# Performance work log

Measured on AMD Instinct MI355X. Metric: run time of the kernel, lower is better.

## Reference

```python
import jax, jax.numpy as jnp
import numpy as np

EPS = 1e-5
L0_BETA = 2.0 / 3.0   # unused in deterministic path
L0_GAMMA = -0.1
L0_ZETA = 1.1
NEG_SLOPE = 0.2


def _bn(v, axes, g, b, pshape):
    # batch-norm using batch statistics (training-mode math, biased var like torch)
    mean = jnp.mean(v, axis=axes, keepdims=True)
    var = jnp.var(v, axis=axes, keepdims=True)
    return (v - mean) * jax.lax.rsqrt(var + EPS) * g.reshape(pshape) + b.reshape(pshape)


def setup_inputs() -> dict:
    key = jax.random.key(0)
    ks = jax.random.split(key, 4)
    n, c, t, h, w = 32, 1024, 32, 7, 7
    n_nodes = 128
    return {
        "x": jax.random.normal(ks[0], (n, c, t, h, w), jnp.float32),
        "nodes": jax.random.normal(ks[1], (n_nodes, c), jnp.float32),
        "g1": jnp.ones((c,), jnp.float32), "b1": jnp.zeros((c,), jnp.float32),
        "g2": jnp.ones((c,), jnp.float32), "b2": jnp.zeros((c,), jnp.float32),
        "g3": jnp.ones((n_nodes,), jnp.float32), "b3": jnp.zeros((n_nodes,), jnp.float32),
        "W": jax.random.normal(ks[2], (c, c), jnp.float32) * (1.0 / np.sqrt(c)),
        "bW": jnp.zeros((c,), jnp.float32),
        "loc": jnp.ones((1,), jnp.float32),  # hard-concrete location param (penalty_loc_mean=1)
        "g6": jnp.ones((c,), jnp.float32), "b6": jnp.zeros((c,), jnp.float32),
    }


def reference(x, nodes, g1, b1, g2, b2, g3, b3, W, bW, loc, g6, b6):
    # x: (n,c,t,h,w), nodes: (K,c)
    # bn_1: BatchNorm3d over channel c
    x = _bn(x, (0, 2, 3, 4), g1, b1, (1, -1, 1, 1, 1))
    # bn_2: BatchNorm1d on (K,c) -> per-channel stats across nodes
    nd = _bn(nodes, (0,), g2, b2, (1, -1))
    # linear_1
    nd = nd @ W.T + bW
    # bn_3: pl.BatchNorm(n_nodes, dim=0) -> per-node stats across channels
    nd = _bn(nd, (1,), g3, b3, (-1, 1))
    # tensor_product_1: f (n,h,w,K,t)
    f = jnp.einsum('ncthw,kc->nhwkt', x, nd)
    # L0Norm hard-concrete gate (deterministic/eval path)
    s_bar = jax.nn.sigmoid(loc) * (L0_ZETA - L0_GAMMA) + L0_GAMMA
    gate = jnp.clip(s_bar, 0.0, 1.0)
    alpha = f * gate
    # tensor_product_2: y (n,c,t,h,w)
    y = jnp.einsum('nhwkt,kc->ncthw', alpha, nd)
    # bn_6 + LeakyReLU(0.2)
    y = _bn(y, (0, 2, 3, 4), g6, b6, (1, -1, 1, 1, 1))
    return jnp.where(y >= 0, y, NEG_SLOPE * y)
```

## Files before the change

kernel.cpp:

```cpp
#include <hip/hip_runtime.h>
#include <hip/hip_bf16.h>

#define NB 32
#define CC 1024
#define SS 1568
#define KK 128
#define NCOL 448
#define EPSV 1e-5f
#define XP_P 132
#define NSB3 224

typedef __attribute__((ext_vector_type(8))) short bf16x8;
typedef __attribute__((ext_vector_type(4))) short bf16x4v;
typedef __attribute__((ext_vector_type(4))) float f32x4;

__device__ __forceinline__ unsigned short f2bf(float f) {
  union { float f; unsigned u; } v; v.f = f;
  return (unsigned short)((v.u + 0x7fffu + ((v.u >> 16) & 1u)) >> 16);
}
__device__ __forceinline__ float bf2f(unsigned short h) {
  union { unsigned u; float f; } v; v.u = ((unsigned)h) << 16; return v.f;
}

__global__ __launch_bounds__(256) void xpose_stats(
    const float* __restrict__ x, unsigned short* __restrict__ xT,
    float* __restrict__ p1s, float* __restrict__ p1q) {
  __shared__ float lt[64 * XP_P];
  int sb = blockIdx.x, cc = blockIdx.y, n = blockIdx.z;
  int t = threadIdx.x;
  int s0 = sb * 112, c0 = cc * 64;
  const float* xp = x + ((size_t)n * CC + c0) * SS + s0;
  #pragma unroll
  for (int j = 0; j < 7; j++) {
    int idx = t + 256 * j;
    int r = idx / 28, q = idx % 28;
    float4 v = *(const float4*)(xp + (size_t)r * SS + 4 * q);
    *(float4*)&lt[r * XP_P + 4 * (q ^ (r >> 3))] = v;
  }
  __syncthreads();
  {
    int r = t >> 2, m = t & 3;
    float s = 0.f, sq = 0.f;
    #pragma unroll
    for (int i = 0; i < 7; i++) {
      int b = m * 7 + i;
      float4 v = *(const float4*)&lt[r * XP_P + 4 * (b ^ (r >> 3))];
      s  += v.x + v.y + v.z + v.w;
      sq += v.x * v.x + v.y * v.y + v.z * v.z + v.w * v.w;
    }
    s += __shfl_xor(s, 1); sq += __shfl_xor(sq, 1);
    s += __shfl_xor(s, 2); sq += __shfl_xor(sq, 2);
    if (m == 0) {
      int col = n * 14 + sb;
      p1s[(size_t)(c0 + r) * NCOL + col] = s;
      p1q[(size_t)(c0 + r) * NCOL + col] = sq;
    }
  }
  if (t < 224) {
    int co = t & 7, sl = t >> 3;
    #pragma unroll
    for (int j = 0; j < 4; j++) {
      int sloc = sl + 28 * j;
      int s = s0 + sloc;
      bf16x8 pk;
      #pragma unroll
      for (int i = 0; i < 8; i++) {
        int r = co * 8 + i;
        pk[i] = (short)f2bf(lt[r * XP_P + 4 * ((sloc >> 2) ^ co) + (sloc & 3)]);
      }
      size_t off = (size_t)n * 1605632 +
                   (size_t)((s >> 4) * 32 + (cc * 2 + (co >> 2))) * 512 +
                   (s & 15) * 32 + (co & 3) * 8;
      *(bf16x8*)(xT + off) = pk;
    }
  }
}

__global__ void bn1_fin(const float* __restrict__ p1s, const float* __restrict__ p1q,
                        const float* __restrict__ g1, const float* __restrict__ b1,
                        float* a1, float* c1) {
  __shared__ float red[4][32][2];
  int t = threadIdx.x;
  int cl = t & 31, part = t >> 5, w = t >> 6;
  int c = blockIdx.x * 32 + cl;
  const float4* ps = (const float4*)(p1s + (size_t)c * NCOL + part * 56);
  const float4* pq = (const float4*)(p1q + (size_t)c * NCOL + part * 56);
  float s = 0.f, sq = 0.f;
  #pragma unroll
  for (int i = 0; i < 14; i++) {
    float4 v = ps[i]; s += v.x + v.y + v.z + v.w;
    float4 u = pq[i]; sq += u.x + u.y + u.z + u.w;
  }
  s += __shfl_xor(s, 32); sq += __shfl_xor(sq, 32);
  if ((t & 63) < 32) { red[w][cl][0] = s; red[w][cl][1] = sq; }
  __syncthreads();
  if (t < 32) {
    float st = red[0][t][0] + red[1][t][0] + red[2][t][0] + red[3][t][0];
    float qt = red[0][t][1] + red[1][t][1] + red[2][t][1] + red[3][t][1];
    float inv = 1.f / ((float)NB * SS);
    float m = st * inv, var = qt * inv - m * m;
    float r = rsqrtf(var + EPSV);
    float a = g1[c] * r;
    a1[c] = a; c1[c] = b1[c] - m * a;
  }
}

__global__ void bn2_nh(const float* __restrict__ nodes, const float* __restrict__ g2,
                       const float* __restrict__ b2, unsigned short* __restrict__ nh) {
  __shared__ float sred[4][8][2];
  __shared__ float bc[8][2];
  int t = threadIdx.x;
  int cl = t & 7, kq = t >> 3, w = t >> 6;
  int c = blockIdx.x * 8 + cl;
  float s = 0.f, sq = 0.f;
  #pragma unroll
  for (int i = 0; i < 4; i++) {
    float v = nodes[(size_t)(kq + 32 * i) * CC + c];
    s += v; sq += v * v;
  }
  s += __shfl_xor(s, 8);  sq += __shfl_xor(sq, 8);
  s += __shfl_xor(s, 16); sq += __shfl_xor(sq, 16);
  s += __shfl_xor(s, 32); sq += __shfl_xor(sq, 32);
  if ((t & 63) < 8) { sred[w][cl][0] = s; sred[w][cl][1] = sq; }
  __syncthreads();
  if (t < 8) {
    float st = sred[0][t][0] + sred[1][t][0] + sred[2][t][0] + sred[3][t][0];
    float qt = sred[0][t][1] + sred[1][t][1] + sred[2][t][1] + sred[3][t][1];
    float inv = 1.f / (float)KK;
    float m = st * inv, var = qt * inv - m * m;
    float r = rsqrtf(var + EPSV);
    float a = g2[blockIdx.x * 8 + t] * r;
    bc[t][0] = a; bc[t][1] = b2[blockIdx.x * 8 + t] - m * a;
  }
  __syncthreads();
  float a = bc[cl][0], cc2 = bc[cl][1];
  #pragma unroll
  for (int i = 0; i < 4; i++) {
    int k = kq + 32 * i;
    nh[(size_t)k * CC + c] = f2bf(nodes[(size_t)k * CC + c] * a + cc2);
  }
}

__global__ __launch_bounds__(256) void linear_mfma(
    const unsigned short* __restrict__ nh, const float* __restrict__ Wm,
    const float* __restrict__ bW, float* __restrict__ Lb) {
  int jt = blockIdx.x, mt = blockIdx.y;
  int t = threadIdx.x, w = t >> 6, lane = t & 63, g = lane >> 4, l15 = lane & 15;
  int krow = mt * 64 + w * 16 + l15;
  f32x4 acc[2];
  acc[0] = (f32x4){0.f,0.f,0.f,0.f}; acc[1] = (f32x4){0.f,0.f,0.f,0.f};
  #pragma unroll 4
  for (int c0 = 0; c0 < CC; c0 += 32) {
    bf16x8 af = *(const bf16x8*)(nh + (size_t)krow * CC + c0 + g * 8);
    #pragma unroll
    for (int nf = 0; nf < 2; nf++) {
      const float* wr = Wm + (size_t)(jt * 32 + nf * 16 + l15) * CC + c0 + g * 8;
      float4 v0 = *(const float4*)wr, v1 = *(const float4*)(wr + 4);
      bf16x8 bfr;
      bfr[0] = (short)f2bf(v0.x); bfr[1] = (short)f2bf(v0.y);
      bfr[2] = (short)f2bf(v0.z); bfr[3] = (short)f2bf(v0.w);
      bfr[4] = (short)f2bf(v1.x); bfr[5] = (short)f2bf(v1.y);
      bfr[6] = (short)f2bf(v1.z); bfr[7] = (short)f2bf(v1.w);
      acc[nf] = __builtin_amdgcn_mfma_f32_16x16x32_bf16(af, bfr, acc[nf], 0, 0, 0);
    }
  }
  #pragma unroll
  for (int nf = 0; nf < 2; nf++) {
    int j = jt * 32 + nf * 16 + l15;
    float bwv = bW[j];
    #pragma unroll
    for (int r = 0; r < 4; r++)
      Lb[(size_t)(mt * 64 + w * 16 + g * 4 + r) * CC + j] = acc[nf][r] + bwv;
  }
}

__global__ void bn3_pack(const float* __restrict__ Lb, const float* __restrict__ g3,
                         const float* __restrict__ b3, const float* __restrict__ loc,
                         const float* __restrict__ a1, const float* __restrict__ c1,
                         unsigned short* __restrict__ ndA2, unsigned short* __restrict__ Mt,
                         unsigned short* __restrict__ MtL, float* __restrict__ Cst) {
  __shared__ float red[8];
  int k = blockIdx.x, t = threadIdx.x, w = t >> 6;
  float vv[4];
  float s = 0.f, sq = 0.f;
  for (int i = 0; i < 4; i++) {
    float v = Lb[(size_t)k * CC + t + 256 * i];
    vv[i] = v; s += v; sq += v * v;
  }
  for (int m = 1; m < 64; m <<= 1) { s += __shfl_xor(s, m); sq += __shfl_xor(sq, m); }
  if ((t & 63) == 0) { red[w] = s; red[4 + w] = sq; }
  __syncthreads();
  s  = red[0] + red[1] + red[2] + red[3];
  sq = red[4] + red[5] + red[6] + red[7];
  float inv = 1.f / (float)CC;
  float m3 = s * inv, var = sq * inv - m3 * m3;
  float r = rsqrtf(var + EPSV);
  float a = g3[k] * r, cc3 = b3[k] - m3 * a;
  float lv = loc[0];
  float gate = 1.f / (1.f + __expf(-lv)) * 1.2f - 0.1f;
  gate = fminf(fmaxf(gate, 0.f), 1.f);
  float cs = 0.f;
  for (int i = 0; i < 4; i++) {
    int j = t + 256 * i;
    float nd = vv[i] * a + cc3;
    unsigned short ndb = f2bf(nd * a1[j]);
    unsigned short mtb = f2bf(gate * nd);
    ndA2[(size_t)((k >> 4) * 32 + (j >> 5)) * 512 + (k & 15) * 32 + ((j >> 3) & 3) * 8 + (j & 7)] = ndb;
    Mt[(size_t)((j >> 4) * 4 + (k >> 5)) * 512 + (j & 15) * 32 + ((k >> 3) & 3) * 8 + (k & 7)] = mtb;
    MtL[(size_t)j * KK + k] = mtb;
    cs += c1[j] * nd;
  }
  for (int m = 1; m < 64; m <<= 1) cs += __shfl_xor(cs, m);
  __syncthreads();
  if ((t & 63) == 0) red[w] = cs;
  __syncthreads();
  if (t == 0) Cst[k] = red[0] + red[1] + red[2] + red[3];
}

__global__ __launch_bounds__(256) void gemm1(
    const unsigned short* __restrict__ ndA2, const unsigned short* __restrict__ xT,
    const float* __restrict__ Cst, unsigned short* __restrict__ GT) {
  int sb = blockIdx.x;
  int n  = blockIdx.y;
  int t = threadIdx.x, w = t >> 6, lane = t & 63, g = lane >> 4, l15 = lane & 15;
  f32x4 acc[2][2];
  for (int m = 0; m < 2; m++)
    for (int nf = 0; nf < 2; nf++) acc[m][nf] = (f32x4){0.f, 0.f, 0.f, 0.f};
  int lofs = l15 * 32 + g * 8;
  const unsigned short* xb = xT + (size_t)n * 1605632;
  #pragma unroll 4
  for (int cc2 = 0; cc2 < 32; cc2++) {
    bf16x8 af[2], bfr[2];
    #pragma unroll
    for (int m = 0; m < 2; m++)
      af[m] = *(const bf16x8*)(ndA2 + (size_t)((w * 2 + m) * 32 + cc2) * 512 + lofs);
    #pragma unroll
    for (int nf = 0; nf < 2; nf++)
      bfr[nf] = *(const bf16x8*)(xb + (size_t)((sb * 2 + nf) * 32 + cc2) * 512 + lofs);
    #pragma unroll
    for (int m = 0; m < 2; m++)
      #pragma unroll
      for (int nf = 0; nf < 2; nf++)
        acc[m][nf] = __builtin_amdgcn_mfma_f32_16x16x32_bf16(af[m], bfr[nf], acc[m][nf], 0, 0, 0);
  }
  unsigned short* gtn = GT + (size_t)n * 200704;
  #pragma unroll
  for (int nf = 0; nf < 2; nf++) {
    #pragma unroll
    for (int m = 0; m < 2; m++) {
      int kb = w * 32 + m * 16 + g * 4;
      float4 cst = *(const float4*)(Cst + kb);
      bf16x4v ov;
      ov[0] = (short)f2bf(acc[m][nf][0] + cst.x);
      ov[1] = (short)f2bf(acc[m][nf][1] + cst.y);
      ov[2] = (short)f2bf(acc[m][nf][2] + cst.z);
      ov[3] = (short)f2bf(acc[m][nf][3] + cst.w);
      int g2 = m * 2 + (g >> 1);
      int e0 = (g & 1) * 4;
      *(bf16x4v*)(gtn + (size_t)((sb * 2 + nf) * 4 + w) * 512 + l15 * 32 + g2 * 8 + e0) = ov;
    }
  }
}

__global__ __launch_bounds__(256) void gram(const unsigned short* __restrict__ GT,
                                            float* __restrict__ part) {
  __shared__ unsigned short lds[112 * 128];
  int b = blockIdx.x, t = threadIdx.x;
  int k1b = t >> 4, k2b = t & 15;
  float acc[8][8];
  float gsum[8];
  #pragma unroll
  for (int i = 0; i < 8; i++) {
    gsum[i] = 0.f;
    #pragma unroll
    for (int j = 0; j < 8; j++) acc[i][j] = 0.f;
  }
  for (int chunk = 0; chunk < 2; chunk++) {
    int St0 = b * 14 + chunk * 7;
    #pragma unroll
    for (int it = 0; it < 7; it++) {
      int u = t + 256 * it;
      int Stl = u >> 8, rem = u & 255;
      bf16x8 v = *(const bf16x8*)(GT + (size_t)(St0 + Stl) * 2048 + rem * 8);
      int sl = Stl * 16 + ((rem & 63) >> 2);
      int kk = (rem >> 6) * 32 + (rem & 3) * 8;
      *(bf16x8*)&lds[sl * 128 + kk] = v;
    }
    __syncthreads();
    for (int sl = 0; sl < 112; sl++) {
      bf16x8 A8 = *(const bf16x8*)&lds[sl * 128 + k1b * 8];
      bf16x8 B8 = *(const bf16x8*)&lds[sl * 128 + k2b * 8];
      float a[8], bb[8];
      #pragma unroll
      for (int i = 0; i < 8; i++) { a[i] = bf2f((unsigned short)A8[i]); bb[i] = bf2f((unsigned short)B8[i]); }
      #pragma unroll
      for (int i = 0; i < 8; i++)
        #pragma unroll
        for (int j = 0; j < 8; j++) acc[i][j] += a[i] * bb[j];
      if (k1b == 0) {
        #pragma unroll
        for (int j = 0; j < 8; j++) gsum[j] += bb[j];
      }
    }
    __syncthreads();
  }
  float* pb = part + (size_t)b * 16512;
  #pragma unroll
  for (int i = 0; i < 8; i++) {
    int k1 = k1b * 8 + i;
    *(float4*)(pb + k1 * 128 + k2b * 8)     = (float4){acc[i][0], acc[i][1], acc[i][2], acc[i][3]};
    *(float4*)(pb + k1 * 128 + k2b * 8 + 4) = (float4){acc[i][4], acc[i][5], acc[i][6], acc[i][7]};
  }
  if (k1b == 0) {
    *(float4*)(pb + 16384 + k2b * 8)     = (float4){gsum[0], gsum[1], gsum[2], gsum[3]};
    *(float4*)(pb + 16384 + k2b * 8 + 4) = (float4){gsum[4], gsum[5], gsum[6], gsum[7]};
  }
}

__global__ void gram_reduce(const float* __restrict__ part, float* __restrict__ Cov) {
  int e = blockIdx.x * 256 + threadIdx.x;
  if (e >= 16512) return;
  float s = 0.f;
  #pragma unroll 8
  for (int p = 0; p < NSB3; p++) s += part[(size_t)p * 16512 + e];
  Cov[e] = s;
}

__global__ __launch_bounds__(256) void bn6stats(
    const float* __restrict__ Cov, const unsigned short* __restrict__ MtL,
    const float* __restrict__ g6, const float* __restrict__ b6,
    float* a6, float* c6) {
  __shared__ float covL[16384];
  __shared__ float mL[8 * 128];
  __shared__ float gbL[128];
  int b = blockIdx.x, t = threadIdx.x;
  int c0 = b * 8;
  #pragma unroll
  for (int i = 0; i < 16; i++) {
    int u = t + 256 * i;
    *(float4*)&covL[u * 4] = *(const float4*)(Cov + u * 4);
  }
  if (t < 128) {
    int row = t >> 4, unit = t & 15;
    bf16x8 v = *(const bf16x8*)(MtL + (size_t)(c0 + row) * KK + unit * 8);
    #pragma unroll
    for (int j = 0; j < 8; j++) mL[row * 128 + unit * 8 + j] = bf2f((unsigned short)v[j]);
  }
  if (t < 32) *(float4*)&gbL[t * 4] = *(const float4*)(Cov + 16384 + t * 4);
  __syncthreads();
  int cl = t >> 5, kq = t & 31;
  float4 m4 = *(const float4*)&mL[cl * 128 + kq * 4];
  float4 g4 = *(const float4*)&gbL[kq * 4];
  float mv = m4.x * g4.x + m4.y * g4.y + m4.z * g4.z + m4.w * g4.w;
  float vv = 0.f;
  for (int k = 0; k < 128; k++) {
    float4 c4 = *(const float4*)&covL[k * 128 + kq * 4];
    float mk = mL[cl * 128 + k];
    vv += mk * (c4.x * m4.x + c4.y * m4.y + c4.z * m4.z + c4.w * m4.w);
  }
  for (int msk = 1; msk < 32; msk <<= 1) { mv += __shfl_xor(mv, msk); vv += __shfl_xor(vv, msk); }
  if (kq == 0) {
    int c = c0 + cl;
    float inv = 1.f / ((float)NB * SS);
    float mean = mv * inv, var = vv * inv - mean * mean;
    float r = rsqrtf(var + EPSV);
    float a = g6[c] * r;
    a6[c] = a; c6[c] = b6[c] - mean * a;
  }
}

__global__ __launch_bounds__(256) void gemm2(
    const unsigned short* __restrict__ Mt, const unsigned short* __restrict__ GT,
    const float* __restrict__ a6, const float* __restrict__ c6,
    float* __restrict__ out) {
  int ct = blockIdx.x;
  int sb = blockIdx.y;
  int n  = blockIdx.z;
  int t = threadIdx.x, w = t >> 6, lane = t & 63, g = lane >> 4, l15 = lane & 15;
  f32x4 acc[2][7];
  for (int m = 0; m < 2; m++)
    for (int nf = 0; nf < 7; nf++) acc[m][nf] = (f32x4){0.f, 0.f, 0.f, 0.f};
  int lofs = l15 * 32 + g * 8;
  const unsigned short* gtb = GT + (size_t)n * 200704;
  #pragma unroll
  for (int ks = 0; ks < 4; ks++) {
    bf16x8 af[2];
    #pragma unroll
    for (int m = 0; m < 2; m++)
      af[m] = *(const bf16x8*)(Mt + (size_t)((ct * 8 + w * 2 + m) * 4 + ks) * 512 + lofs);
    #pragma unroll
    for (int nf = 0; nf < 7; nf++) {
      bf16x8 bfr = *(const bf16x8*)(gtb + (size_t)((sb * 7 + nf) * 4 + ks) * 512 + lofs);
      #pragma unroll
      for (int m = 0; m < 2; m++)
        acc[m][nf] = __builtin_amdgcn_mfma_f32_16x16x32_bf16(af[m], bfr, acc[m][nf], 0, 0, 0);
    }
  }
  #pragma unroll
  for (int m = 0; m < 2; m++) {
    int cb = ct * 128 + w * 32 + m * 16 + g * 4;
    float4 av = *(const float4*)(a6 + cb);
    float4 cv = *(const float4*)(c6 + cb);
    #pragma unroll
    for (int nf = 0; nf < 7; nf++) {
      int s = sb * 112 + nf * 16 + l15;
      #pragma unroll
      for (int r = 0; r < 4; r++) {
        float a = (r == 0) ? av.x : (r == 1) ? av.y : (r == 2) ? av.z : av.w;
        float cc = (r == 0) ? cv.x : (r == 1) ? cv.y : (r == 2) ? cv.z : cv.w;
        float v = acc[m][nf][r] * a + cc;
        v = v >= 0.f ? v : 0.2f * v;
        out[((size_t)(n * CC + cb + r)) * SS + s] = v;
      }
    }
  }
}

extern "C" void kernel_launch(void* const* d_in, const int* in_sizes, int n_in,
                              void* d_out, int out_size, void* d_ws, size_t ws_size,
                              hipStream_t stream) {
  const float* x     = (const float*)d_in[0];
  const float* nodes = (const float*)d_in[1];
  const float* g1 = (const float*)d_in[2];
  const float* b1 = (const float*)d_in[3];
  const float* g2 = (const float*)d_in[4];
  const float* b2 = (const float*)d_in[5];
  const float* g3 = (const float*)d_in[6];
  const float* b3 = (const float*)d_in[7];
  const float* Wm = (const float*)d_in[8];
  const float* bW = (const float*)d_in[9];
  const float* loc = (const float*)d_in[10];
  const float* g6 = (const float*)d_in[11];
  const float* b6 = (const float*)d_in[12];
  float* out = (float*)d_out;
  char* ws = (char*)d_ws;

  float* p1s = (float*)(ws + 0);
  float* p1q = (float*)(ws + 1835008);
  float* a1  = (float*)(ws + 3670016);
  float* c1  = (float*)(ws + 3674112);
  float* Cst = (float*)(ws + 3678208);
  unsigned short* nh   = (unsigned short*)(ws + 3682304);
  float* Lb  = (float*)(ws + 3944448);
  unsigned short* ndA2 = (unsigned short*)(ws + 4468736);
  unsigned short* Mt   = (unsigned short*)(ws + 4730880);
  unsigned short* MtL  = (unsigned short*)(ws + 4993024);
  float* a6  = (float*)(ws + 5255168);
  float* c6  = (float*)(ws + 5259264);
  float* Cov = (float*)(ws + 5263360);
  float* gramP = (float*)(ws + 5329920);
  unsigned short* GT = (unsigned short*)(ws + 20124672);
  unsigned short* xT = (unsigned short*)(ws + 32969728);

  xpose_stats<<<dim3(14, 16, NB), dim3(256), 0, stream>>>(x, xT, p1s, p1q);
  bn2_nh<<<dim3(128), dim3(256), 0, stream>>>(nodes, g2, b2, nh);
  linear_mfma<<<dim3(32, 2), dim3(256), 0, stream>>>(nh, Wm, bW, Lb);
  bn1_fin<<<dim3(32), dim3(256), 0, stream>>>(p1s, p1q, g1, b1, a1, c1);
  bn3_pack<<<dim3(KK), dim3(256), 0, stream>>>(Lb, g3, b3, loc, a1, c1, ndA2, Mt, MtL, Cst);
  gemm1<<<dim3(49, NB), dim3(256), 0, stream>>>(ndA2, xT, Cst, GT);
  gram<<<dim3(NSB3), dim3(256), 0, stream>>>(GT, gramP);
  gram_reduce<<<dim3(65), dim3(256), 0, stream>>>(gramP, Cov);
  bn6stats<<<dim3(128), dim3(256), 0, stream>>>(Cov, MtL, g6, b6, a6, c6);
  gemm2<<<dim3(8, 14, NB), dim3(256), 0, stream>>>(Mt, GT, a6, c6, out);
}
```

Baseline: 298.8 us.

## Retune transpose block size, fp32 gram LDS, split reduction, XCD-swizzled gemm2

Several unrelated changes land together. xpose_stats now runs with 512 threads per block, and gram stores fp32 in LDS so the inner loop no longer converts bf16. gram_reduce is split into two stages to get more parallelism. gemm2 uses a 1D grid swizzled across XCDs so blocks sharing GT data land on the same XCD, and it writes the output with nontemporal stores. gram's LDS footprint doubles to 56KB, which may lower occupancy, and there is one extra kernel launch.

```diff
diff --git a/kernel.cpp b/kernel.cpp
--- a/kernel.cpp
+++ b/kernel.cpp
@@ -22,7 +22,7 @@
   union { unsigned u; float f; } v; v.u = ((unsigned)h) << 16; return v.f;
 }
 
-__global__ __launch_bounds__(256) void xpose_stats(
+__global__ __launch_bounds__(512) void xpose_stats(
     const float* __restrict__ x, unsigned short* __restrict__ xT,
     float* __restrict__ p1s, float* __restrict__ p1q) {
   __shared__ float lt[64 * XP_P];
@@ -31,14 +31,16 @@
   int s0 = sb * 112, c0 = cc * 64;
   const float* xp = x + ((size_t)n * CC + c0) * SS + s0;
   #pragma unroll
-  for (int j = 0; j < 7; j++) {
-    int idx = t + 256 * j;
-    int r = idx / 28, q = idx % 28;
-    float4 v = *(const float4*)(xp + (size_t)r * SS + 4 * q);
-    *(float4*)&lt[r * XP_P + 4 * (q ^ (r >> 3))] = v;
-  }
-  __syncthreads();
-  {
+  for (int j = 0; j < 4; j++) {
+    int idx = t + 512 * j;
+    if (idx < 1792) {
+      int r = idx / 28, q = idx % 28;
+      float4 v = *(const float4*)(xp + (size_t)r * SS + 4 * q);
+      *(float4*)&lt[r * XP_P + 4 * (q ^ (r >> 3))] = v;
+    }
+  }
+  __syncthreads();
+  if (t < 256) {
     int r = t >> 2, m = t & 3;
     float s = 0.f, sq = 0.f;
     #pragma unroll
@@ -56,11 +58,11 @@
       p1q[(size_t)(c0 + r) * NCOL + col] = sq;
     }
   }
-  if (t < 224) {
+  if (t < 448) {
     int co = t & 7, sl = t >> 3;
     #pragma unroll
-    for (int j = 0; j < 4; j++) {
-      int sloc = sl + 28 * j;
+    for (int j = 0; j < 2; j++) {
+      int sloc = sl + 56 * j;
       int s = s0 + sloc;
       bf16x8 pk;
       #pragma unroll
@@ -264,7 +266,7 @@
 
 __global__ __launch_bounds__(256) void gram(const unsigned short* __restrict__ GT,
                                             float* __restrict__ part) {
-  __shared__ unsigned short lds[112 * 128];
+  __shared__ float lf[112 * 128];
   int b = blockIdx.x, t = threadIdx.x;
   int k1b = t >> 4, k2b = t & 15;
   float acc[8][8];
@@ -284,15 +286,22 @@
       bf16x8 v = *(const bf16x8*)(GT + (size_t)(St0 + Stl) * 2048 + rem * 8);
       int sl = Stl * 16 + ((rem & 63) >> 2);
       int kk = (rem >> 6) * 32 + (rem & 3) * 8;
-      *(bf16x8*)&lds[sl * 128 + kk] = v;
+      float4 f0, f1;
+      f0.x = bf2f((unsigned short)v[0]); f0.y = bf2f((unsigned short)v[1]);
+      f0.z = bf2f((unsigned short)v[2]); f0.w = bf2f((unsigned short)v[3]);
+      f1.x = bf2f((unsigned short)v[4]); f1.y = bf2f((unsigned short)v[5]);
+      f1.z = bf2f((unsigned short)v[6]); f1.w = bf2f((unsigned short)v[7]);
+      *(float4*)&lf[sl * 128 + kk] = f0;
+      *(float4*)&lf[sl * 128 + kk + 4] = f1;
     }
     __syncthreads();
     for (int sl = 0; sl < 112; sl++) {
-      bf16x8 A8 = *(const bf16x8*)&lds[sl * 128 + k1b * 8];
-      bf16x8 B8 = *(const bf16x8*)&lds[sl * 128 + k2b * 8];
-      float a[8], bb[8];
-      #pragma unroll
-      for (int i = 0; i < 8; i++) { a[i] = bf2f((unsigned short)A8[i]); bb[i] = bf2f((unsigned short)B8[i]); }
+      float4 a0 = *(const float4*)&lf[sl * 128 + k1b * 8];
+      float4 a1 = *(const float4*)&lf[sl * 128 + k1b * 8 + 4];
+      float4 b0 = *(const float4*)&lf[sl * 128 + k2b * 8];
+      float4 b1 = *(const float4*)&lf[sl * 128 + k2b * 8 + 4];
+      float a[8]  = {a0.x, a0.y, a0.z, a0.w, a1.x, a1.y, a1.z, a1.w};
+      float bb[8] = {b0.x, b0.y, b0.z, b0.w, b1.x, b1.y, b1.z, b1.w};
       #pragma unroll
       for (int i = 0; i < 8; i++)
         #pragma unroll
@@ -317,13 +326,19 @@
   }
 }
 
-__global__ void gram_reduce(const float* __restrict__ part, float* __restrict__ Cov) {
+__global__ void gram_reduceA(const float* __restrict__ part, float* __restrict__ partB) {
   int e = blockIdx.x * 256 + threadIdx.x;
   if (e >= 16512) return;
+  int p0 = blockIdx.y * 56;
   float s = 0.f;
   #pragma unroll 8
-  for (int p = 0; p < NSB3; p++) s += part[(size_t)p * 16512 + e];
-  Cov[e] = s;
+  for (int p = p0; p < p0 + 56; p++) s += part[(size_t)p * 16512 + e];
+  partB[(size_t)blockIdx.y * 16512 + e] = s;
+}
+__global__ void gram_reduceB(const float* __restrict__ partB, float* __restrict__ Cov) {
+  int e = blockIdx.x * 256 + threadIdx.x;
+  if (e >= 16512) return;
+  Cov[e] = partB[e] + partB[16512 + e] + partB[2 * 16512 + e] + partB[3 * 16512 + e];
 }
 
 __global__ __launch_bounds__(256) void bn6stats(
@@ -373,9 +388,12 @@
     const unsigned short* __restrict__ Mt, const unsigned short* __restrict__ GT,
     const float* __restrict__ a6, const float* __restrict__ c6,
     float* __restrict__ out) {
-  int ct = blockIdx.x;
-  int sb = blockIdx.y;
-  int n  = blockIdx.z;
+  int id = blockIdx.x;
+  int xcd = id & 7;
+  int mid = id >> 3;
+  int ct  = mid & 7;
+  int p   = (mid >> 3) * 8 + xcd;
+  int sb  = p % 14, n = p / 14;
   int t = threadIdx.x, w = t >> 6, lane = t & 63, g = lane >> 4, l15 = lane & 15;
   f32x4 acc[2][7];
   for (int m = 0; m < 2; m++)
@@ -410,7 +428,7 @@
         float cc = (r == 0) ? cv.x : (r == 1) ? cv.y : (r == 2) ? cv.z : cv.w;
         float v = acc[m][nf][r] * a + cc;
         v = v >= 0.f ? v : 0.2f * v;
-        out[((size_t)(n * CC + cb + r)) * SS + s] = v;
+        __builtin_nontemporal_store(v, &out[((size_t)(n * CC + cb + r)) * SS + s]);
       }
     }
   }
@@ -451,15 +469,17 @@
   float* gramP = (float*)(ws + 5329920);
   unsigned short* GT = (unsigned short*)(ws + 20124672);
   unsigned short* xT = (unsigned short*)(ws + 32969728);
-
-  xpose_stats<<<dim3(14, 16, NB), dim3(256), 0, stream>>>(x, xT, p1s, p1q);
+  float* partB = (float*)(ws + 135730176);
+
+  xpose_stats<<<dim3(14, 16, NB), dim3(512), 0, stream>>>(x, xT, p1s, p1q);
   bn2_nh<<<dim3(128), dim3(256), 0, stream>>>(nodes, g2, b2, nh);
   linear_mfma<<<dim3(32, 2), dim3(256), 0, stream>>>(nh, Wm, bW, Lb);
   bn1_fin<<<dim3(32), dim3(256), 0, stream>>>(p1s, p1q, g1, b1, a1, c1);
   bn3_pack<<<dim3(KK), dim3(256), 0, stream>>>(Lb, g3, b3, loc, a1, c1, ndA2, Mt, MtL, Cst);
   gemm1<<<dim3(49, NB), dim3(256), 0, stream>>>(ndA2, xT, Cst, GT);
   gram<<<dim3(NSB3), dim3(256), 0, stream>>>(GT, gramP);
-  gram_reduce<<<dim3(65), dim3(256), 0, stream>>>(gramP, Cov);
+  gram_reduceA<<<dim3(65, 4), dim3(256), 0, stream>>>(gramP, partB);
+  gram_reduceB<<<dim3(65), dim3(256), 0, stream>>>(partB, Cov);
   bn6stats<<<dim3(128), dim3(256), 0, stream>>>(Cov, MtL, g6, b6, a6, c6);
-  gemm2<<<dim3(8, 14, NB), dim3(256), 0, stream>>>(Mt, GT, a6, c6, out);
-}
+  gemm2<<<dim3(3584), dim3(256), 0, stream>>>(Mt, GT, a6, c6, out);
+}
```

Result: faster. 278.1 us (-6.9%).
